# Kernel optimization log

Measured on AMD Instinct MI355X. Metric: run time of the kernel, lower is better.

## Reference

```python
import jax, jax.numpy as jnp
import numpy as np

EMBED = 2048
HEADS = 16
HEAD_DIM = EMBED // HEADS


def setup_inputs() -> dict:
    key = jax.random.key(0)
    ks = jax.random.split(key, 9)
    s = 1.0 / np.sqrt(EMBED)
    inp = {"x": jax.random.normal(ks[0], (2, 2048, EMBED), dtype=jnp.float32)}
    for i, name in enumerate(["q", "k", "v", "o"]):
        inp[f"W{name}"] = jax.random.uniform(ks[1 + 2 * i], (EMBED, EMBED), dtype=jnp.float32, minval=-s, maxval=s)
        inp[f"b{name}"] = jax.random.uniform(ks[2 + 2 * i], (EMBED,), dtype=jnp.float32, minval=-s, maxval=s)
    return inp


def reference(x, Wq, bq, Wk, bk, Wv, bv, Wo, bo):
    B, S, E = x.shape
    def split_heads(t):
        return t.reshape(B, S, HEADS, HEAD_DIM).transpose(0, 2, 1, 3)  # [B,H,S,D]
    q = split_heads(x @ Wq.T + bq)
    k = split_heads(x @ Wk.T + bk)
    v = split_heads(x @ Wv.T + bv)
    scale = 1.0 / np.sqrt(HEAD_DIM)
    scores = jnp.einsum("bhqd,bhkd->bhqk", q, k) * scale  # [B,H,S,S]
    causal = jnp.tril(jnp.ones((S, S), dtype=bool))
    scores = jnp.where(causal[None, None], scores, -jnp.inf)
    attn = jax.nn.softmax(scores, axis=-1)
    out = jnp.einsum("bhqk,bhkd->bhqd", attn, v)  # [B,H,S,D]
    out = out.transpose(0, 2, 1, 3).reshape(B, S, E)
    return out @ Wo.T + bo
```

## Files before the change

kernel.cpp:

```cpp
#include <hip/hip_runtime.h>

typedef unsigned short u16;
typedef unsigned int u32;
typedef __attribute__((ext_vector_type(8))) short bf16x8;
typedef __attribute__((ext_vector_type(4))) float f32x4;

#define MFMA(a, b, c) __builtin_amdgcn_mfma_f32_16x16x32_bf16((a), (b), (c), 0, 0, 0)

__device__ inline u16 f2bf(float f) {
  u32 u = __float_as_uint(f);
  u = (u + 0x7fffu + ((u >> 16) & 1u)) >> 16;
  return (u16)u;
}

__device__ inline void gld16(u16* lds, const u16* g) {
  __builtin_amdgcn_global_load_lds((const __attribute__((address_space(1))) void*)g,
                                   (__attribute__((address_space(3))) void*)lds,
                                   16, 0, 0);
}

__global__ __launch_bounds__(256) void cvt_all(const float* __restrict__ x,
                                               const float* __restrict__ wa,
                                               const float* __restrict__ wb,
                                               const float* __restrict__ wc,
                                               const float* __restrict__ wd,
                                               uint2* __restrict__ dst) {
  int i = blockIdx.x * 256 + threadIdx.x;
  const float* s;
  int off;
  if (i < 2097152) {
    s = x; off = i;
  } else {
    int j = i - 2097152;
    int which = j >> 20;
    off = j & 1048575;
    s = (which == 0) ? wa : (which == 1) ? wb : (which == 2) ? wc : wd;
  }
  float4 f = ((const float4*)s)[off];
  u32 lo = (u32)f2bf(f.x) | ((u32)f2bf(f.y) << 16);
  u32 hi = (u32)f2bf(f.z) | ((u32)f2bf(f.w) << 16);
  dst[i] = make_uint2(lo, hi);
}

__device__ inline void gemm_core(const u16* __restrict__ A, const u16* __restrict__ W,
                                 u16* As, u16* Bs, int m0, int n0, f32x4 acc[4][4]) {
  const int K = 2048;
  int t = threadIdx.x, w = t >> 6, l = t & 63;
  int rowL = w * 16 + (l >> 2);
  int colL = (l & 3) * 8;
  const u16* ga = A + (size_t)(m0 + rowL) * K + colL;
  const u16* gb = W + (size_t)(n0 + rowL) * K + colL;
  u16* la = As + w * 512;
  u16* lb = Bs + w * 512;
  int wr = (w >> 1) * 64, wc = (w & 1) * 64;
  int fr = l & 15, fo = (l >> 4) * 8;
  for (int k0 = 0; k0 < K; k0 += 32) {
    gld16(la, ga + k0);
    gld16(la + 2048, ga + (size_t)64 * K + k0);
    gld16(lb, gb + k0);
    gld16(lb + 2048, gb + (size_t)64 * K + k0);
    __syncthreads();
    bf16x8 af[4], bfv[4];
#pragma unroll
    for (int i = 0; i < 4; ++i) af[i] = *(const bf16x8*)&As[(wr + i * 16 + fr) * 32 + fo];
#pragma unroll
    for (int i = 0; i < 4; ++i) bfv[i] = *(const bf16x8*)&Bs[(wc + i * 16 + fr) * 32 + fo];
#pragma unroll
    for (int mi = 0; mi < 4; ++mi)
#pragma unroll
      for (int ni = 0; ni < 4; ++ni)
        acc[mi][ni] = MFMA(af[mi], bfv[ni], acc[mi][ni]);
    __syncthreads();
  }
}

__global__ __launch_bounds__(256) void qkv_gemm(
    const u16* __restrict__ X, const u16* __restrict__ Wq, const u16* __restrict__ Wk,
    const u16* __restrict__ Wv, const float* __restrict__ bq, const float* __restrict__ bk,
    const float* __restrict__ bv, u16* __restrict__ Qo, u16* __restrict__ Ko,
    u16* __restrict__ Vo) {
  __shared__ __attribute__((aligned(16))) u16 As[4096];
  __shared__ __attribute__((aligned(16))) u16 Bs[4096];
  int which = blockIdx.x >> 4;
  int n0 = (blockIdx.x & 15) * 128;
  int m0 = blockIdx.y * 128;
  const u16* W = (which == 0) ? Wq : (which == 1) ? Wk : Wv;
  const float* bias = (which == 0) ? bq : (which == 1) ? bk : bv;
  u16* out = (which == 0) ? Qo : (which == 1) ? Ko : Vo;
  float scale = (which == 0) ? 0.08838834764831845f : 1.0f;
  f32x4 zero4 = {0.f, 0.f, 0.f, 0.f};
  f32x4 acc[4][4];
#pragma unroll
  for (int i = 0; i < 4; ++i)
#pragma unroll
    for (int j = 0; j < 4; ++j) acc[i][j] = zero4;
  gemm_core(X, W, As, Bs, m0, n0, acc);
  int t = threadIdx.x, w = t >> 6, l = t & 63;
  int wr = (w >> 1) * 64, wc = (w & 1) * 64;
  if (which == 2) {
#pragma unroll
    for (int mi = 0; mi < 4; ++mi) {
#pragma unroll
      for (int ni = 0; ni < 4; ++ni) {
        int row = m0 + wr + mi * 16 + (l >> 4) * 4;
        int col = n0 + wc + ni * 16 + (l & 15);
        float bb = bias[col];
        int h = col >> 7, d = col & 127;
        int b = row >> 11, s = row & 2047;
        u32 p0 = (u32)f2bf(acc[mi][ni][0] + bb) | ((u32)f2bf(acc[mi][ni][1] + bb) << 16);
        u32 p1 = (u32)f2bf(acc[mi][ni][2] + bb) | ((u32)f2bf(acc[mi][ni][3] + bb) << 16);
        *(uint2*)&out[((size_t)(b * 16 + h) * 128 + d) * 2048 + s] = make_uint2(p0, p1);
      }
    }
  } else {
#pragma unroll
    for (int mi = 0; mi < 4; ++mi) {
#pragma unroll
      for (int ni = 0; ni < 4; ++ni) {
        int row = m0 + wr + mi * 16 + (l >> 4) * 4;
        int col = n0 + wc + ni * 16 + (l & 15);
        float bb = bias[col];
        int h = col >> 7, d = col & 127;
#pragma unroll
        for (int i = 0; i < 4; ++i) {
          int m = row + i;
          int b = m >> 11, s = m & 2047;
          float v = (acc[mi][ni][i] + bb) * scale;
          out[(((size_t)b * 16 + h) * 2048 + s) * 128 + d] = f2bf(v);
        }
      }
    }
  }
}

__global__ __launch_bounds__(256) void oproj_gemm(const u16* __restrict__ A,
                                                  const u16* __restrict__ W,
                                                  const float* __restrict__ bias,
                                                  float* __restrict__ out) {
  __shared__ __attribute__((aligned(16))) u16 As[4096];
  __shared__ __attribute__((aligned(16))) u16 Bs[4096];
  int n0 = blockIdx.x * 128, m0 = blockIdx.y * 128;
  f32x4 zero4 = {0.f, 0.f, 0.f, 0.f};
  f32x4 acc[4][4];
#pragma unroll
  for (int i = 0; i < 4; ++i)
#pragma unroll
    for (int j = 0; j < 4; ++j) acc[i][j] = zero4;
  gemm_core(A, W, As, Bs, m0, n0, acc);
  int t = threadIdx.x, w = t >> 6, l = t & 63;
  int wr = (w >> 1) * 64, wc = (w & 1) * 64;
#pragma unroll
  for (int mi = 0; mi < 4; ++mi) {
#pragma unroll
    for (int ni = 0; ni < 4; ++ni) {
      int row = m0 + wr + mi * 16 + (l >> 4) * 4;
      int col = n0 + wc + ni * 16 + (l & 15);
      float bb = bias[col];
#pragma unroll
      for (int i = 0; i < 4; ++i) out[(size_t)(row + i) * 2048 + col] = acc[mi][ni][i] + bb;
    }
  }
}

__global__ __launch_bounds__(256, 2) void attn_fwd(const u16* __restrict__ Q,
                                                   const u16* __restrict__ K,
                                                   const u16* __restrict__ Vt,
                                                   u16* __restrict__ AO) {
  __shared__ __attribute__((aligned(16))) u16 Ks[8192];
  __shared__ __attribute__((aligned(16))) u16 Vts[8192];
  __shared__ __attribute__((aligned(16))) u16 Pl[8192];
  const int D = 128;
  int b3 = blockIdx.x;
  int bh = b3 & 31;
  int xq = b3 >> 5;
  int qt = (xq < 8) ? (15 - xq) : (xq - 8);
  int t = threadIdx.x, w = t >> 6, l = t & 63, g = l >> 4, c = l & 15;
  size_t base = (size_t)bh * 2048 * 128;
  const u16* Vbh = Vt + base;
  int q0 = qt * 128;
  int qrw = q0 + w * 32;
  bf16x8 qf[2][4];
#pragma unroll
  for (int mi = 0; mi < 2; ++mi) {
    const u16* qp = Q + base + (size_t)(qrw + mi * 16 + c) * D + g * 8;
#pragma unroll
    for (int ks = 0; ks < 4; ++ks) qf[mi][ks] = *(const bf16x8*)(qp + ks * 32);
  }
  f32x4 zero4 = {0.f, 0.f, 0.f, 0.f};
  f32x4 oacc[2][8];
#pragma unroll
  for (int mi = 0; mi < 2; ++mi)
#pragma unroll
    for (int i = 0; i < 8; ++i) oacc[mi][i] = zero4;
  float mrow[2][4], lrow[2][4];
#pragma unroll
  for (int mi = 0; mi < 2; ++mi)
#pragma unroll
    for (int i = 0; i < 4; ++i) { mrow[mi][i] = -1e30f; lrow[mi][i] = 0.f; }
  char* pw = (char*)(Pl + w * 2048);
  int ktmax = 2 * qt + 1;
  for (int kt = 0; kt <= ktmax; ++kt) {
    int kv0 = kt * 64;
    __syncthreads();
#pragma unroll
    for (int ci = 0; ci < 4; ++ci) {
      int row = w * 16 + ci * 4 + g;
      int cc = c ^ (row & 7);
      gld16(Ks + w * 2048 + ci * 512, K + base + (size_t)(kv0 + row) * D + cc * 8);
    }
#pragma unroll
    for (int ci = 0; ci < 4; ++ci) {
      int vr = ci * 32 + w * 8 + (l >> 3);
      int vslot = (l & 7) ^ ((l >> 3) & 7);
      gld16(Vts + ci * 2048 + w * 512, Vbh + (size_t)vr * 2048 + kv0 + vslot * 8);
    }
    __syncthreads();
    if (kv0 <= qrw + 31) {
      f32x4 sacc[2][4];
#pragma unroll
      for (int mi = 0; mi < 2; ++mi)
#pragma unroll
        for (int n = 0; n < 4; ++n) sacc[mi][n] = zero4;
#pragma unroll
      for (int ks = 0; ks < 4; ++ks) {
#pragma unroll
        for (int n = 0; n < 4; ++n) {
          int row = n * 16 + c;
          bf16x8 kf = *(const bf16x8*)&Ks[row * 128 + (((ks * 4 + g) ^ (c & 7)) << 3)];
          sacc[0][n] = MFMA(qf[0][ks], kf, sacc[0][n]);
          sacc[1][n] = MFMA(qf[1][ks], kf, sacc[1][n]);
        }
      }
      float sc[2][4][4];
#pragma unroll
      for (int mi = 0; mi < 2; ++mi)
#pragma unroll
        for (int n = 0; n < 4; ++n)
#pragma unroll
          for (int i = 0; i < 4; ++i) sc[mi][n][i] = sacc[mi][n][i];
      if (kv0 + 63 > qrw) {
#pragma unroll
        for (int mi = 0; mi < 2; ++mi)
#pragma unroll
          for (int n = 0; n < 4; ++n) {
            int kv = kv0 + n * 16 + c;
#pragma unroll
            for (int i = 0; i < 4; ++i)
              if (kv > qrw + mi * 16 + g * 4 + i) sc[mi][n][i] = -1e30f;
          }
      }
      float tmax[2][4];
#pragma unroll
      for (int mi = 0; mi < 2; ++mi)
#pragma unroll
        for (int i = 0; i < 4; ++i)
          tmax[mi][i] = fmaxf(fmaxf(sc[mi][0][i], sc[mi][1][i]), fmaxf(sc[mi][2][i], sc[mi][3][i]));
#pragma unroll
      for (int x = 1; x < 16; x <<= 1)
#pragma unroll
        for (int mi = 0; mi < 2; ++mi)
#pragma unroll
          for (int i = 0; i < 4; ++i) tmax[mi][i] = fmaxf(tmax[mi][i], __shfl_xor(tmax[mi][i], x));
      float corr[2][4], rs[2][4];
#pragma unroll
      for (int mi = 0; mi < 2; ++mi)
#pragma unroll
        for (int i = 0; i < 4; ++i) {
          float mn = fmaxf(mrow[mi][i], tmax[mi][i]);
          corr[mi][i] = __expf(mrow[mi][i] - mn);
          mrow[mi][i] = mn;
          rs[mi][i] = 0.f;
        }
      float ps[2][4][4];
#pragma unroll
      for (int mi = 0; mi < 2; ++mi)
#pragma unroll
        for (int n = 0; n < 4; ++n)
#pragma unroll
          for (int i = 0; i < 4; ++i) {
            ps[mi][n][i] = __expf(sc[mi][n][i] - mrow[mi][i]);
            rs[mi][i] += ps[mi][n][i];
          }
#pragma unroll
      for (int x = 1; x < 16; x <<= 1)
#pragma unroll
        for (int mi = 0; mi < 2; ++mi)
#pragma unroll
          for (int i = 0; i < 4; ++i) rs[mi][i] += __shfl_xor(rs[mi][i], x);
#pragma unroll
      for (int mi = 0; mi < 2; ++mi)
#pragma unroll
        for (int i = 0; i < 4; ++i) lrow[mi][i] = lrow[mi][i] * corr[mi][i] + rs[mi][i];
#pragma unroll
      for (int mi = 0; mi < 2; ++mi)
#pragma unroll
        for (int nf = 0; nf < 8; ++nf)
#pragma unroll
          for (int i = 0; i < 4; ++i) oacc[mi][nf][i] *= corr[mi][i];
#pragma unroll
      for (int mi = 0; mi < 2; ++mi)
#pragma unroll
        for (int n = 0; n < 4; ++n)
#pragma unroll
          for (int i = 0; i < 4; ++i) {
            int row = mi * 16 + g * 4 + i;
            *(u16*)(pw + row * 128 + ((n * 32 + c * 2) ^ ((row & 7) << 4))) = f2bf(ps[mi][n][i]);
          }
#pragma unroll
      for (int ks = 0; ks < 2; ++ks) {
        bf16x8 pf0 = *(const bf16x8*)(pw + (c)*128 + ((ks * 64 + g * 16) ^ ((c & 7) << 4)));
        bf16x8 pf1 = *(const bf16x8*)(pw + (16 + c) * 128 + ((ks * 64 + g * 16) ^ ((c & 7) << 4)));
#pragma unroll
        for (int nf = 0; nf < 8; ++nf) {
          bf16x8 vf = *(const bf16x8*)&Vts[(nf * 16 + c) * 64 + (((ks * 4 + g) ^ (c & 7)) << 3)];
          oacc[0][nf] = MFMA(pf0, vf, oacc[0][nf]);
          oacc[1][nf] = MFMA(pf1, vf, oacc[1][nf]);
        }
      }
    }
  }
  int b = bh >> 4, h = bh & 15;
#pragma unroll
  for (int mi = 0; mi < 2; ++mi)
#pragma unroll
    for (int nf = 0; nf < 8; ++nf) {
      int d = h * 128 + nf * 16 + c;
#pragma unroll
      for (int i = 0; i < 4; ++i) {
        int q = qrw + mi * 16 + g * 4 + i;
        AO[((size_t)b * 2048 + q) * 2048 + d] = f2bf(oacc[mi][nf][i] / lrow[mi][i]);
      }
    }
}

extern "C" void kernel_launch(void* const* d_in, const int* in_sizes, int n_in,
                              void* d_out, int out_size, void* d_ws, size_t ws_size,
                              hipStream_t stream) {
  const float* x = (const float*)d_in[0];
  const float* Wq = (const float*)d_in[1];
  const float* bq = (const float*)d_in[2];
  const float* Wk = (const float*)d_in[3];
  const float* bk = (const float*)d_in[4];
  const float* Wv = (const float*)d_in[5];
  const float* bv = (const float*)d_in[6];
  const float* Wo = (const float*)d_in[7];
  const float* bo = (const float*)d_in[8];
  float* out = (float*)d_out;

  u16* xb = (u16*)d_ws;
  u16* Wqb = xb + 8388608;
  u16* Wkb = Wqb + 4194304;
  u16* Wvb = Wkb + 4194304;
  u16* Wvb2 = Wvb;
  u16* Wob = Wvb + 4194304;
  u16* Qb = Wob + 4194304;
  u16* Kb = Qb + 8388608;
  u16* Vb = Kb + 8388608;
  u16* AOb = xb;
  (void)Wvb2;

  cvt_all<<<24576, 256, 0, stream>>>(x, Wq, Wk, Wv, Wo, (uint2*)d_ws);
  qkv_gemm<<<dim3(48, 32), 256, 0, stream>>>(xb, Wqb, Wkb, Wvb, bq, bk, bv, Qb, Kb, Vb);
  attn_fwd<<<512, 256, 0, stream>>>(Qb, Kb, Vb, AOb);
  oproj_gemm<<<dim3(16, 32), 256, 0, stream>>>(AOb, Wob, bo, out);
}
```

Measured before the change: 307.0 us.

## Pipeline GEMM tiles through a 4-stage LDS ring with XOR-swizzled layout

The shared GEMM core now uses a four-buffer LDS ring with a prefetch distance of two K-tiles. Asynchronous global-to-LDS loads overlap MFMA work, and the two __syncthreads per step become a single vmcnt wait plus barrier. The LDS column chunks are XOR-swizzled by row on both the load and the fragment-read side to cut bank conflicts. The price is four times more LDS per block, 64KB, which limits occupancy to two blocks per CU as declared by the new launch bounds. Tail iterations reload the last tile redundantly.

```diff
diff --git a/kernel.cpp b/kernel.cpp
--- a/kernel.cpp
+++ b/kernel.cpp
@@ -45,42 +45,66 @@
 __device__ inline void gemm_core(const u16* __restrict__ A, const u16* __restrict__ W,
                                  u16* As, u16* Bs, int m0, int n0, f32x4 acc[4][4]) {
   const int K = 2048;
+  const int NT = 64;
   int t = threadIdx.x, w = t >> 6, l = t & 63;
-  int rowL = w * 16 + (l >> 2);
-  int colL = (l & 3) * 8;
-  const u16* ga = A + (size_t)(m0 + rowL) * K + colL;
-  const u16* gb = W + (size_t)(n0 + rowL) * K + colL;
-  u16* la = As + w * 512;
-  u16* lb = Bs + w * 512;
   int wr = (w >> 1) * 64, wc = (w & 1) * 64;
-  int fr = l & 15, fo = (l >> 4) * 8;
-  for (int k0 = 0; k0 < K; k0 += 32) {
-    gld16(la, ga + k0);
-    gld16(la + 2048, ga + (size_t)64 * K + k0);
-    gld16(lb, gb + k0);
-    gld16(lb + 2048, gb + (size_t)64 * K + k0);
-    __syncthreads();
+  int fr = l & 15, fg = l >> 4;
+  int r0 = t >> 2;
+  int r1 = 64 + r0;
+  int c00 = (t & 3) ^ ((r0 >> 1) & 3);
+  int c01 = (t & 3) ^ ((r1 >> 1) & 3);
+  const u16* gA = A + (size_t)m0 * K;
+  const u16* gB = W + (size_t)n0 * K;
+  size_t a0 = (size_t)r0 * K + c00 * 8;
+  size_t a1 = (size_t)r1 * K + c01 * 8;
+#pragma unroll
+  for (int p = 0; p < 2; ++p) {
+    u16* sa = As + p * 4096;
+    u16* sb = Bs + p * 4096;
+    int kk = p * 32;
+    gld16(sa + w * 512, gA + a0 + kk);
+    gld16(sa + 2048 + w * 512, gA + a1 + kk);
+    gld16(sb + w * 512, gB + a0 + kk);
+    gld16(sb + 2048 + w * 512, gB + a1 + kk);
+  }
+  for (int kt = 0; kt < NT; ++kt) {
+    int kt2 = (kt + 2 < NT) ? (kt + 2) : (NT - 1);
+    u16* sa = As + ((kt + 2) & 3) * 4096;
+    u16* sb = Bs + ((kt + 2) & 3) * 4096;
+    int kk = kt2 * 32;
+    gld16(sa + w * 512, gA + a0 + kk);
+    gld16(sa + 2048 + w * 512, gA + a1 + kk);
+    gld16(sb + w * 512, gB + a0 + kk);
+    gld16(sb + 2048 + w * 512, gB + a1 + kk);
+    asm volatile("s_waitcnt vmcnt(8)\n\ts_barrier" ::: "memory");
+    const u16* ca = As + (kt & 3) * 4096;
+    const u16* cb = Bs + (kt & 3) * 4096;
     bf16x8 af[4], bfv[4];
 #pragma unroll
-    for (int i = 0; i < 4; ++i) af[i] = *(const bf16x8*)&As[(wr + i * 16 + fr) * 32 + fo];
-#pragma unroll
-    for (int i = 0; i < 4; ++i) bfv[i] = *(const bf16x8*)&Bs[(wc + i * 16 + fr) * 32 + fo];
+    for (int i = 0; i < 4; ++i) {
+      int ar = wr + i * 16 + fr;
+      af[i] = *(const bf16x8*)&ca[ar * 32 + ((fg ^ ((ar >> 1) & 3)) << 3)];
+    }
+#pragma unroll
+    for (int i = 0; i < 4; ++i) {
+      int br = wc + i * 16 + fr;
+      bfv[i] = *(const bf16x8*)&cb[br * 32 + ((fg ^ ((br >> 1) & 3)) << 3)];
+    }
 #pragma unroll
     for (int mi = 0; mi < 4; ++mi)
 #pragma unroll
       for (int ni = 0; ni < 4; ++ni)
         acc[mi][ni] = MFMA(af[mi], bfv[ni], acc[mi][ni]);
-    __syncthreads();
-  }
-}
-
-__global__ __launch_bounds__(256) void qkv_gemm(
+  }
+}
+
+__global__ __launch_bounds__(256, 2) void qkv_gemm(
     const u16* __restrict__ X, const u16* __restrict__ Wq, const u16* __restrict__ Wk,
     const u16* __restrict__ Wv, const float* __restrict__ bq, const float* __restrict__ bk,
     const float* __restrict__ bv, u16* __restrict__ Qo, u16* __restrict__ Ko,
     u16* __restrict__ Vo) {
-  __shared__ __attribute__((aligned(16))) u16 As[4096];
-  __shared__ __attribute__((aligned(16))) u16 Bs[4096];
+  __shared__ __attribute__((aligned(16))) u16 As[16384];
+  __shared__ __attribute__((aligned(16))) u16 Bs[16384];
   int which = blockIdx.x >> 4;
   int n0 = (blockIdx.x & 15) * 128;
   int m0 = blockIdx.y * 128;
@@ -133,12 +157,12 @@
   }
 }
 
-__global__ __launch_bounds__(256) void oproj_gemm(const u16* __restrict__ A,
-                                                  const u16* __restrict__ W,
-                                                  const float* __restrict__ bias,
-                                                  float* __restrict__ out) {
-  __shared__ __attribute__((aligned(16))) u16 As[4096];
-  __shared__ __attribute__((aligned(16))) u16 Bs[4096];
+__global__ __launch_bounds__(256, 2) void oproj_gemm(const u16* __restrict__ A,
+                                                     const u16* __restrict__ W,
+                                                     const float* __restrict__ bias,
+                                                     float* __restrict__ out) {
+  __shared__ __attribute__((aligned(16))) u16 As[16384];
+  __shared__ __attribute__((aligned(16))) u16 Bs[16384];
   int n0 = blockIdx.x * 128, m0 = blockIdx.y * 128;
   f32x4 zero4 = {0.f, 0.f, 0.f, 0.f};
   f32x4 acc[4][4];
@@ -351,13 +375,11 @@
   u16* Wqb = xb + 8388608;
   u16* Wkb = Wqb + 4194304;
   u16* Wvb = Wkb + 4194304;
-  u16* Wvb2 = Wvb;
   u16* Wob = Wvb + 4194304;
   u16* Qb = Wob + 4194304;
   u16* Kb = Qb + 8388608;
   u16* Vb = Kb + 8388608;
   u16* AOb = xb;
-  (void)Wvb2;
 
   cvt_all<<<24576, 256, 0, stream>>>(x, Wq, Wk, Wv, Wo, (uint2*)d_ws);
   qkv_gemm<<<dim3(48, 32), 256, 0, stream>>>(xb, Wqb, Wkb, Wvb, bq, bk, bv, Qb, Kb, Vb);
```

New measurement: 289.5 us. -5.7%, faster.
